# Kernel optimization log

Hardware: AMD Instinct MI355X
Metric: run time of the kernel (lower is better)

The kernel has to match this reference:

```python
import jax, jax.numpy as jnp
import numpy as np

B, N, E = 4, 10000, 160000
F_EXOG = 8
IN_DIM = 9          # 1 (pm25) + F_EXOG
HIST, PRED = 8, 12
HID = 64
GNN_OUT = 13
E_HID, E_OUT = 32, 30
GRU_IN = IN_DIM + GNN_OUT  # 22


def setup_inputs() -> dict:
    key = jax.random.key(0)
    ks = jax.random.split(key, 16)
    s = 0.1
    return {
        "pm25_hist": jax.random.normal(ks[0], (B, HIST, N, 1), jnp.float32),
        "feature": jax.random.normal(ks[1], (B, HIST + PRED, N, F_EXOG), jnp.float32),
        "edge_attr": jax.random.uniform(ks[2], (E, 2), jnp.float32),
        "wind_mean": jnp.array([2.0, 180.0], jnp.float32),
        "wind_std": jnp.array([1.5, 90.0], jnp.float32),
        # edge MLP: Linear(21->32), Sigmoid, Linear(32->30), Sigmoid
        "e_w1": jax.random.normal(ks[3], (2 * IN_DIM + 3, E_HID), jnp.float32) * s,
        "e_b1": jnp.zeros((E_HID,), jnp.float32),
        "e_w2": jax.random.normal(ks[4], (E_HID, E_OUT), jnp.float32) * s,
        "e_b2": jnp.zeros((E_OUT,), jnp.float32),
        # node MLP: Linear(30->13), Sigmoid
        "n_w": jax.random.normal(ks[5], (E_OUT, GNN_OUT), jnp.float32) * s,
        "n_b": jnp.zeros((GNN_OUT,), jnp.float32),
        # GRUCell(22 -> 64), torch layout: weight_ih (3H, in), weight_hh (3H, H)
        "gru_wi": jax.random.normal(ks[6], (3 * HID, GRU_IN), jnp.float32) * s,
        "gru_wh": jax.random.normal(ks[7], (3 * HID, HID), jnp.float32) * s,
        "gru_bi": jnp.zeros((3 * HID,), jnp.float32),
        "gru_bh": jnp.zeros((3 * HID,), jnp.float32),
        # fc_out: Linear(64 -> 1)
        "fc_w": jax.random.normal(ks[8], (HID, 1), jnp.float32) * s,
        "fc_b": jnp.zeros((1,), jnp.float32),
        "edge_index": jax.random.randint(ks[9], (2, E), 0, N, jnp.int64),
    }


def _forward(pm25_hist, feature, edge_attr, wind_mean, wind_std,
             e_w1, e_b1, e_w2, e_b2, n_w, n_b,
             gru_wi, gru_wh, gru_bi, gru_bh, fc_w, fc_b, edge_index):
    batch, _, n_nodes, _ = pm25_hist.shape
    src, tgt = edge_index[0], edge_index[1]

    # buffers precomputed in __init__ (torch.std uses ddof=1)
    edge_mean = edge_attr.mean(axis=0, keepdims=True)
    edge_std = jnp.maximum(jnp.std(edge_attr, axis=0, ddof=1, keepdims=True), 1e-6)
    edge_attr_norm = (edge_attr - edge_mean) / edge_std          # (E, 2)
    city_dist = jnp.maximum(edge_attr[:, 0], 1e-3)               # (E,)
    city_direc = edge_attr[:, 1]                                 # (E,)
    w_std = jnp.maximum(wind_std, 1e-6)

    def graph_gnn(x):                                            # x: (B, N, IN_DIM)
        node_src = x[:, src]                                     # (B, E, IN_DIM)
        node_tgt = x[:, tgt]
        wind = node_src[..., -2:] * w_std + wind_mean            # de-normalize
        speed = jnp.maximum(wind[..., 0], 0.0)                   # (B, E)
        wdir = jnp.deg2rad(wind[..., 1])
        theta = jnp.abs(city_direc - wdir)
        edge_w = jax.nn.relu(3.0 * speed * jnp.cos(theta) / city_dist)  # (B, E)
        ean = jnp.broadcast_to(edge_attr_norm, (x.shape[0], E, 2))
        h = jnp.concatenate([node_src, node_tgt, ean, edge_w[..., None]], axis=-1)
        h = jax.nn.sigmoid(h @ e_w1 + e_b1)
        h = jax.nn.sigmoid(h @ e_w2 + e_b2)                      # (B, E, E_OUT)
        agg = jnp.zeros((x.shape[0], n_nodes, E_OUT), x.dtype)
        agg = agg.at[:, tgt].add(h).at[:, src].add(-h)           # scatter add / sub
        return jax.nn.sigmoid(agg @ n_w + n_b)                   # (B, N, GNN_OUT)

    def gru_step(h, x):                                          # h,x: (B*N, .)
        gi = x @ gru_wi.T + gru_bi
        gh = h @ gru_wh.T + gru_bh
        i_r, i_z, i_n = jnp.split(gi, 3, axis=-1)
        h_r, h_z, h_n = jnp.split(gh, 3, axis=-1)
        r = jax.nn.sigmoid(i_r + h_r)
        z = jax.nn.sigmoid(i_z + h_z)
        n = jnp.tanh(i_n + r * h_n)
        return (1.0 - z) * n + z * h

    def step(carry, feat_t):
        hn, xn = carry                                           # (B*N,HID), (B,N,1)
        x = jnp.concatenate([xn, feat_t], axis=-1)               # (B, N, IN_DIM)
        x_gnn = graph_gnn(x)
        xc = jnp.concatenate([x_gnn, x], axis=-1).reshape(batch * n_nodes, -1)
        hn = gru_step(hn, xc)
        xn = hn.reshape(batch, n_nodes, HID) @ fc_w + fc_b       # (B, N, 1)
        return (hn, xn), xn[..., 0]

    hn0 = jnp.zeros((batch * n_nodes, HID), pm25_hist.dtype)
    xn0 = pm25_hist[:, -1]                                       # (B, N, 1)
    feats = jnp.swapaxes(feature[:, HIST:HIST + PRED], 0, 1)     # (PRED, B, N, F)
    _, preds = jax.lax.scan(step, (hn0, xn0), feats)             # (PRED, B, N)
    return jnp.transpose(preds, (1, 2, 0))                       # (B, N, PRED)


def reference(pm25_hist, feature, edge_attr, wind_mean, wind_std,
              e_w1, e_b1, e_w2, e_b2, n_w, n_b,
              gru_wi, gru_wh, gru_bi, gru_bh, fc_w, fc_b, edge_index):
    return _forward(pm25_hist, feature, edge_attr, wind_mean, wind_std,
                    e_w1, e_b1, e_w2, e_b2, n_w, n_b,
                    gru_wi, gru_wh, gru_bi, gru_bh, fc_w, fc_b, edge_index)
```

## Files before the change

### kernel.cpp

```cpp
#include <hip/hip_runtime.h>
#include <hip/hip_fp16.h>
#include <cstddef>

#define BB    4
#define NN    10000
#define EE    160000
#define BN    40000
#define HISTC 8
#define PREDC 12
#define TSTEP 20
#define FEX   8
#define HIDC  64
#define EHID  32
#define EOUTC 30
#define GOUTC 13
#define GINC  22

typedef float v2f __attribute__((ext_vector_type(2)));
typedef _Float16 v2h __attribute__((ext_vector_type(2)));
typedef _Float16 v8h __attribute__((ext_vector_type(8)));
typedef float f32x4 __attribute__((ext_vector_type(4)));

__device__ __forceinline__ float fast_rcp(float x) { return __builtin_amdgcn_rcpf(x); }
__device__ __forceinline__ float sigm(float x) {
    return fast_rcp(1.0f + __expf(-x));
}
__device__ __forceinline__ v2f sigm2(v2f x) {
    v2f r; r.x = sigm(x.x); r.y = sigm(x.y); return r;
}
__device__ __forceinline__ float tanh_fast(float x) {
    x = fminf(fmaxf(x, -15.0f), 15.0f);
    float e = __expf(2.0f * x);
    return (e - 1.0f) * fast_rcp(e + 1.0f);
}

__device__ __forceinline__ float dot2(__half2 a, __half2 b, float c) {
#if __has_builtin(__builtin_amdgcn_fdot2)
    union { __half2 h; v2h v; } ua, ub;
    ua.h = a; ub.h = b;
    return __builtin_amdgcn_fdot2(ua.v, ub.v, c, false);
#else
    float2 fa = __half22float2(a), fb = __half22float2(b);
    return c + fa.x * fb.x + fa.y * fb.y;
#endif
}

__global__ __launch_bounds__(256) void stats1_kernel(const float* __restrict__ ea,
                                                     double* __restrict__ part) {
    __shared__ double sm[256][4];
    int tid = threadIdx.x;
    double s0 = 0, s1 = 0, q0 = 0, q1 = 0;
    for (int e = blockIdx.x * 256 + tid; e < EE; e += 256 * 256) {
        float2 v = reinterpret_cast<const float2*>(ea)[e];
        double v0 = (double)v.x, v1 = (double)v.y;
        s0 += v0; q0 += v0 * v0;
        s1 += v1; q1 += v1 * v1;
    }
    sm[tid][0] = s0; sm[tid][1] = s1; sm[tid][2] = q0; sm[tid][3] = q1;
    __syncthreads();
    for (int off = 128; off > 0; off >>= 1) {
        if (tid < off)
            for (int k = 0; k < 4; k++) sm[tid][k] += sm[tid + off][k];
        __syncthreads();
    }
    if (tid == 0) {
        part[blockIdx.x * 4 + 0] = sm[0][0];
        part[blockIdx.x * 4 + 1] = sm[0][1];
        part[blockIdx.x * 4 + 2] = sm[0][2];
        part[blockIdx.x * 4 + 3] = sm[0][3];
    }
}

__global__ __launch_bounds__(256) void stats2_kernel(const double* __restrict__ part,
                                                     float* __restrict__ stats) {
    __shared__ double sm[256][4];
    int tid = threadIdx.x;
    sm[tid][0] = part[tid * 4 + 0];
    sm[tid][1] = part[tid * 4 + 1];
    sm[tid][2] = part[tid * 4 + 2];
    sm[tid][3] = part[tid * 4 + 3];
    __syncthreads();
    for (int off = 128; off > 0; off >>= 1) {
        if (tid < off)
            for (int k = 0; k < 4; k++) sm[tid][k] += sm[tid + off][k];
        __syncthreads();
    }
    if (tid == 0) {
        double m0 = sm[0][0] / EE, m1 = sm[0][1] / EE;
        double v0 = (sm[0][2] - sm[0][0] * sm[0][0] / EE) / (double)(EE - 1);
        double v1 = (sm[0][3] - sm[0][1] * sm[0][1] / EE) / (double)(EE - 1);
        float sd0 = fmaxf((float)sqrt(v0 > 0 ? v0 : 0.0), 1e-6f);
        float sd1 = fmaxf((float)sqrt(v1 > 0 ? v1 : 0.0), 1e-6f);
        stats[0] = (float)m0; stats[1] = (float)m1;
        stats[2] = 1.0f / sd0; stats[3] = 1.0f / sd1;
    }
}

__global__ __launch_bounds__(256) void edgepre_kernel(
    const float* __restrict__ ea, const float* __restrict__ stats,
    const int* __restrict__ eidx,
    int* __restrict__ deg_t, int* __restrict__ deg_s,
    float4* __restrict__ epre4)
{
    int e = blockIdx.x * 256 + threadIdx.x;
    if (e >= EE) return;
    float2 v = reinterpret_cast<const float2*>(ea)[e];
    float4 r;
    r.x = (v.x - stats[0]) * stats[2];
    r.y = (v.y - stats[1]) * stats[3];
    r.z = 1.0f / fmaxf(v.x, 1e-3f);
    r.w = v.y;
    epre4[e] = r;
    atomicAdd(&deg_s[eidx[e]], 1);
    atomicAdd(&deg_t[eidx[EE + e]], 1);
}

__global__ __launch_bounds__(256) void cvtw_kernel(
    const float* __restrict__ wi, const float* __restrict__ wh,
    const float* __restrict__ ew2, const float* __restrict__ eb2,
    const float* __restrict__ nw,
    __half* __restrict__ wi_h, __half* __restrict__ wh_h,
    __half* __restrict__ w2b, __half* __restrict__ nwb)
{
    int i = blockIdx.x * 256 + threadIdx.x;
    if (i < 192 * GINC) wi_h[i] = __float2half(wi[i]);
    if (i < 192 * HIDC) wh_h[i] = __float2half(wh[i]);
    if (i < 32 * 32) {
        int o = i >> 5, k = i & 31;
        w2b[i] = (o < EOUTC) ? __float2half(ew2[k * EOUTC + o]) : __half(0.0f);
    }
    if (i < 16 * 32) {
        int j = i >> 5, o = i & 31;
        nwb[i] = (j < GOUTC && o < EOUTC) ? __float2half(nw[o * GOUTC + j])
                                          : __half(0.0f);
    }
}

__global__ void initxn_kernel(const float* __restrict__ pm, float* __restrict__ xn) {
    int i = blockIdx.x * 256 + threadIdx.x;
    if (i >= BN) return;
    int b = i / NN, n = i - b * NN;
    xn[i] = pm[(b * HISTC + (HISTC - 1)) * NN + n];
}

__global__ __launch_bounds__(1024) void scan_kernel(
    const int* __restrict__ deg_t, const int* __restrict__ deg_s,
    int* __restrict__ off_t, int* __restrict__ off_s,
    int* __restrict__ cnt_t, int* __restrict__ cnt_s)
{
    __shared__ int pt[1024], ps[1024];
    int tid = threadIdx.x;
    int base = tid * 10;
    int st = 0, ss = 0;
    for (int k = 0; k < 10; k++) {
        int i = base + k;
        if (i < NN) { st += deg_t[i]; ss += deg_s[i]; }
    }
    pt[tid] = st; ps[tid] = ss;
    __syncthreads();
    for (int off = 1; off < 1024; off <<= 1) {
        int vt = (tid >= off) ? pt[tid - off] : 0;
        int vs = (tid >= off) ? ps[tid - off] : 0;
        __syncthreads();
        pt[tid] += vt; ps[tid] += vs;
        __syncthreads();
    }
    int ext = (tid == 0) ? 0 : pt[tid - 1];
    int exs = (tid == 0) ? 0 : ps[tid - 1];
    for (int k = 0; k < 10; k++) {
        int i = base + k;
        if (i < NN) {
            off_t[i] = ext; cnt_t[i] = ext;
            off_s[i] = exs; cnt_s[i] = exs;
            ext += deg_t[i]; exs += deg_s[i];
        }
    }
    if (tid == 0) { off_t[NN] = EE; off_s[NN] = EE; }
}

__global__ void fillperm_kernel(const int* __restrict__ eidx,
                                const float4* __restrict__ epre4,
                                int* __restrict__ cnt_t, int* __restrict__ cnt_s,
                                int4* __restrict__ eT, float4* __restrict__ epreT)
{
    int e = blockIdx.x * 256 + threadIdx.x;
    if (e >= EE) return;
    int s = eidx[e];
    int g = eidx[EE + e];
    int pt = atomicAdd(&cnt_t[g], 1);
    int ps = atomicAdd(&cnt_s[s], 1);
    int4 r; r.x = s; r.y = g; r.z = ps; r.w = 0;
    eT[pt] = r;
    epreT[pt] = epre4[e];
}

__global__ __launch_bounds__(256) void pre_kernel(
    float* __restrict__ xncur, const float* __restrict__ feature, int t,
    const float* __restrict__ xp,
    const float* __restrict__ fb,
    const float* __restrict__ ew1,
    const float* __restrict__ wmean, const float* __restrict__ wstd,
    __half* __restrict__ preS, __half* __restrict__ preT,
    float2* __restrict__ wind2, float* __restrict__ out)
{
    __shared__ alignas(16) float w1s[18 * EHID];
    for (int i = threadIdx.x; i < 18 * EHID; i += 256) w1s[i] = ew1[i];
    __syncthreads();
    int idx = blockIdx.x * 256 + threadIdx.x;
    if (idx >= BN * 8) return;
    int i = idx >> 3;
    int c = idx & 7;
    int b = i / NN, n = i - b * NN;
    float x0;
    if (t == 0) {
        x0 = xncur[i];
    } else {
        x0 = (xp[i] + xp[BN + i]) + (xp[2 * BN + i] + xp[3 * BN + i]) + fb[0];
        if (c == 0) {
            xncur[i] = x0;
            out[(size_t)i * PREDC + (t - 1)] = x0;
        }
    }
    float x[9];
    x[0] = x0;
    {
        const float4* fp = reinterpret_cast<const float4*>(
            feature + (((size_t)b * TSTEP + HISTC + t) * NN + n) * FEX);
        float4 u = fp[0], v = fp[1];
        x[1] = u.x; x[2] = u.y; x[3] = u.z; x[4] = u.w;
        x[5] = v.x; x[6] = v.y; x[7] = v.z; x[8] = v.w;
    }
    float4 aS = {0.f, 0.f, 0.f, 0.f}, aT = {0.f, 0.f, 0.f, 0.f};
    #pragma unroll
    for (int k = 0; k < 9; k++) {
        float4 wS = reinterpret_cast<const float4*>(&w1s[k * EHID])[c];
        float4 wT = reinterpret_cast<const float4*>(&w1s[(9 + k) * EHID])[c];
        aS.x += x[k] * wS.x; aS.y += x[k] * wS.y; aS.z += x[k] * wS.z; aS.w += x[k] * wS.w;
        aT.x += x[k] * wT.x; aT.y += x[k] * wT.y; aT.z += x[k] * wT.z; aT.w += x[k] * wT.w;
    }
    union { uint2 u; __half h[4]; } sv, tv;
    sv.h[0] = __float2half(aS.x); sv.h[1] = __float2half(aS.y);
    sv.h[2] = __float2half(aS.z); sv.h[3] = __float2half(aS.w);
    tv.h[0] = __float2half(aT.x); tv.h[1] = __float2half(aT.y);
    tv.h[2] = __float2half(aT.z); tv.h[3] = __float2half(aT.w);
    reinterpret_cast<uint2*>(preS + (size_t)i * EHID)[c] = sv.u;
    reinterpret_cast<uint2*>(preT + (size_t)i * EHID)[c] = tv.u;
    if (c == 1) {
        float sd0 = fmaxf(wstd[0], 1e-6f), sd1 = fmaxf(wstd[1], 1e-6f);
        float speed = fmaxf(x[7] * sd0 + wmean[0], 0.f);
        float wdir  = (x[8] * sd1 + wmean[1]) * 0.017453292519943295f;
        float2 wv; wv.x = 3.0f * speed; wv.y = wdir;
        wind2[i] = wv;
    }
}

__global__ __launch_bounds__(256) void finalout_kernel(
    const float* __restrict__ xp, const float* __restrict__ fb,
    float* __restrict__ out)
{
    int i = blockIdx.x * 256 + threadIdx.x;
    if (i >= BN) return;
    out[(size_t)i * PREDC + (PREDC - 1)] =
        (xp[i] + xp[BN + i]) + (xp[2 * BN + i] + xp[3 * BN + i]) + fb[0];
}

#define H1STR 40
#define S2STR 36
#define H3STR 20
__global__ __launch_bounds__(256) void edge_kernel(
    const int4* __restrict__ eT, const float4* __restrict__ epreT,
    const __half* __restrict__ preS, const __half* __restrict__ preT,
    const float2* __restrict__ wind2,
    const float* __restrict__ ew1, const float* __restrict__ eb1,
    const __half* __restrict__ w2b, const __half* __restrict__ nwb,
    const float* __restrict__ eb2,
    __half* __restrict__ h3t, __half* __restrict__ h3s)
{
    __shared__ alignas(16) __half h1s[256 * H1STR];
    __shared__ alignas(16) __half s2s[4][16 * S2STR];
    __shared__ alignas(16) __half h3x[256 * H3STR];

    int tid  = threadIdx.x;
    int lane = tid & 63, wv = tid >> 6;
    int l15  = lane & 15, lk = lane >> 4;
    int i = blockIdx.x * 256 + tid;
    int b = blockIdx.y;
    int4 et = eT[i];
    int s = et.x, g = et.y, ps = et.z;
    float4 ep = epreT[i];

    size_t iS = (size_t)b * NN + s, iT = (size_t)b * NN + g;
    float2 wvd = wind2[iS];
    float ew = fmaxf(wvd.x * __cosf(fabsf(ep.w - wvd.y)) * ep.z, 0.f);

    v8h bw2a, bw2b, bnw;
    {
        union { uint4 u; v8h h; } t;
        t.u = *reinterpret_cast<const uint4*>(w2b + l15 * 32 + lk * 8);        bw2a = t.h;
        t.u = *reinterpret_cast<const uint4*>(w2b + (16 + l15) * 32 + lk * 8); bw2b = t.h;
        t.u = *reinterpret_cast<const uint4*>(nwb + l15 * 32 + lk * 8);        bnw  = t.h;
    }
    float b2v0 = eb2[l15];
    float b2v1 = eb2[(16 + l15) < EOUTC ? (16 + l15) : (EOUTC - 1)];

    union alignas(16) { uint4 u[4]; __half2 h2[16]; } RS, RT;
    {
        const uint4* p;
        p = reinterpret_cast<const uint4*>(preS + iS * EHID);
        RS.u[0] = p[0]; RS.u[1] = p[1]; RS.u[2] = p[2]; RS.u[3] = p[3];
        p = reinterpret_cast<const uint4*>(preT + iT * EHID);
        RT.u[0] = p[0]; RT.u[1] = p[1]; RT.u[2] = p[2]; RT.u[3] = p[3];
    }

    const v2f* W18 = reinterpret_cast<const v2f*>(ew1 + 18 * EHID);
    const v2f* W19 = reinterpret_cast<const v2f*>(ew1 + 19 * EHID);
    const v2f* W20 = reinterpret_cast<const v2f*>(ew1 + 20 * EHID);
    const v2f* B1  = reinterpret_cast<const v2f*>(eb1);
    float ean0 = ep.x, ean1 = ep.y;
    union alignas(16) { uint4 u[4]; __half2 h2[16]; } H1;
    #pragma unroll
    for (int q = 0; q < 16; q++) {
        v2f u = W18[q] * ean0 + W19[q] * ean1 + B1[q] + W20[q] * ew;
        float2 rs = __half22float2(RS.h2[q]);
        float2 rt = __half22float2(RT.h2[q]);
        u.x += rs.x + rt.x;
        u.y += rs.y + rt.y;
        v2f sg = sigm2(u);
        H1.h2[q] = __floats2half2_rn(sg.x, sg.y);
    }
    {
        uint4* dst = reinterpret_cast<uint4*>(h1s + tid * H1STR);
        dst[0] = H1.u[0]; dst[1] = H1.u[1]; dst[2] = H1.u[2]; dst[3] = H1.u[3];
    }

    f32x4 zero = {0.f, 0.f, 0.f, 0.f};
    __half* s2w = s2s[wv];
    #pragma unroll
    for (int mt = 0; mt < 4; ++mt) {
        v8h af;
        {
            union { uint4 u; v8h h; } t;
            t.u = *reinterpret_cast<const uint4*>(
                h1s + (wv * 64 + mt * 16 + l15) * H1STR + lk * 8);
            af = t.h;
        }
        f32x4 a0 = __builtin_amdgcn_mfma_f32_16x16x32_f16(af, bw2a, zero, 0, 0, 0);
        f32x4 a1 = __builtin_amdgcn_mfma_f32_16x16x32_f16(af, bw2b, zero, 0, 0, 0);
        #pragma unroll
        for (int q = 0; q < 4; ++q) {
            int rl = lk * 4 + q;
            s2w[rl * S2STR + l15]      = __float2half(sigm(a0[q] + b2v0));
            s2w[rl * S2STR + 16 + l15] = __float2half(sigm(a1[q] + b2v1));
        }
        v8h a2;
        {
            union { uint2 u[2]; v8h h; } t;
            const __half* p2 = s2w + l15 * S2STR + lk * 8;
            t.u[0] = *reinterpret_cast<const uint2*>(p2);
            t.u[1] = *reinterpret_cast<const uint2*>(p2 + 4);
            a2 = t.h;
        }
        f32x4 h3a = __builtin_amdgcn_mfma_f32_16x16x32_f16(a2, bnw, zero, 0, 0, 0);
        #pragma unroll
        for (int q = 0; q < 4; ++q) {
            h3x[(wv * 64 + mt * 16 + lk * 4 + q) * H3STR + l15] = __float2half(h3a[q]);
        }
    }

    union alignas(16) { uint4 u4[2]; uint2 u[4]; } R;
    {
        const uint2* hp = reinterpret_cast<const uint2*>(h3x + tid * H3STR);
        R.u[0] = hp[0]; R.u[1] = hp[1]; R.u[2] = hp[2]; R.u[3] = hp[3];
    }
    {
        __half* oT = h3t + ((size_t)b * EE + i) * 16;
        reinterpret_cast<uint4*>(oT)[0] = R.u4[0];
        reinterpret_cast<uint4*>(oT)[1] = R.u4[1];
        __half* oS = h3s + ((size_t)b * EE + ps) * 16;
        reinterpret_cast<uint4*>(oS)[0] = R.u4[0];
        reinterpret_cast<uint4*>(oS)[1] = R.u4[1];
    }
}

__global__ __launch_bounds__(256) void gather_kernel(
    const __half* __restrict__ h3t, const __half* __restrict__ h3s,
    const int* __restrict__ off_t, const int* __restrict__ off_s,
    const float* __restrict__ nb, const float* __restrict__ xncur,
    __half* __restrict__ xcagg)
{
    int n = (blockIdx.x * 256 + threadIdx.x) >> 6;
    if (n >= NN) return;
    n = __builtin_amdgcn_readfirstlane(n);
    int lane = threadIdx.x & 63;
    int b   = lane >> 4;
    int e4  = (lane >> 2) & 3;
    int chq = lane & 3;

    const __half* ht = h3t + (size_t)b * ((size_t)EE * 16) + chq * 4;
    const __half* hs = h3s + (size_t)b * ((size_t)EE * 16) + chq * 4;

    float a0 = 0.f, a1 = 0.f, a2 = 0.f, a3 = 0.f;
    {
        int i0 = off_t[n], i1 = off_t[n + 1];
        for (int i = i0 + e4; i < i1; i += 4) {
            uint2 v = *reinterpret_cast<const uint2*>(ht + (size_t)i * 16);
            float2 f01 = __half22float2(*reinterpret_cast<__half2*>(&v.x));
            float2 f23 = __half22float2(*reinterpret_cast<__half2*>(&v.y));
            a0 += f01.x; a1 += f01.y; a2 += f23.x; a3 += f23.y;
        }
    }
    {
        int i0 = off_s[n], i1 = off_s[n + 1];
        for (int i = i0 + e4; i < i1; i += 4) {
            uint2 v = *reinterpret_cast<const uint2*>(hs + (size_t)i * 16);
            float2 f01 = __half22float2(*reinterpret_cast<__half2*>(&v.x));
            float2 f23 = __half22float2(*reinterpret_cast<__half2*>(&v.y));
            a0 -= f01.x; a1 -= f01.y; a2 -= f23.x; a3 -= f23.y;
        }
    }
    a0 += __shfl_xor(a0, 4); a1 += __shfl_xor(a1, 4);
    a2 += __shfl_xor(a2, 4); a3 += __shfl_xor(a3, 4);
    a0 += __shfl_xor(a0, 8); a1 += __shfl_xor(a1, 8);
    a2 += __shfl_xor(a2, 8); a3 += __shfl_xor(a3, 8);

    if (e4 == 0) {
        int c0 = chq * 4;
        float nb0 = nb[c0 < GOUTC ? c0 : GOUTC - 1];
        float nb1 = nb[c0 + 1 < GOUTC ? c0 + 1 : GOUTC - 1];
        float nb2 = nb[c0 + 2 < GOUTC ? c0 + 2 : GOUTC - 1];
        float nb3 = nb[c0 + 3 < GOUTC ? c0 + 3 : GOUTC - 1];
        float v0 = (c0 + 0 < GOUTC) ? sigm(a0 + nb0) : 0.f;
        float v1 = (c0 + 1 < GOUTC) ? sigm(a1 + nb1)
                 : ((c0 + 1 == GOUTC) ? xncur[(size_t)b * NN + n] : 0.f);
        float v2 = (c0 + 2 < GOUTC) ? sigm(a2 + nb2) : 0.f;
        float v3 = (c0 + 3 < GOUTC) ? sigm(a3 + nb3) : 0.f;
        union { uint2 u; __half h[4]; } o;
        o.h[0] = __float2half(v0); o.h[1] = __float2half(v1);
        o.h[2] = __float2half(v2); o.h[3] = __float2half(v3);
        *reinterpret_cast<uint2*>(xcagg + ((size_t)b * NN + n) * 16 + c0) = o.u;
    }
}

__global__ __launch_bounds__(256) void node_kernel(
    const __half* __restrict__ xcagg, const float* __restrict__ feature, int t,
    const __half* __restrict__ wi_h, const __half* __restrict__ wh_h,
    const float* __restrict__ bi, const float* __restrict__ bh,
    const float* __restrict__ fw,
    const __half2* __restrict__ hnold, __half2* __restrict__ hnnew,
    float* __restrict__ xp)
{
    __shared__ float xpart[4][64];
    int lane = threadIdx.x & 63;
    int wav  = threadIdx.x >> 6;
    int jb   = blockIdx.y;
    int node = blockIdx.x * 64 + lane;
    int b = node / NN;
    int n = node - b * NN;

    __half2 xch[11];
    {
        union alignas(16) { uint4 u[2]; __half2 h2[8]; } X;
        const uint4* xp16 = reinterpret_cast<const uint4*>(xcagg + (size_t)node * 16);
        X.u[0] = xp16[0]; X.u[1] = xp16[1];
        #pragma unroll
        for (int p = 0; p < 7; p++) xch[p] = X.h2[p];
    }
    {
        const float4* fp = reinterpret_cast<const float4*>(
            feature + (((size_t)b * TSTEP + HISTC + t) * NN + n) * FEX);
        float4 u = fp[0], v = fp[1];
        xch[7]  = __floats2half2_rn(u.x, u.y);
        xch[8]  = __floats2half2_rn(u.z, u.w);
        xch[9]  = __floats2half2_rn(v.x, v.y);
        xch[10] = __floats2half2_rn(v.z, v.w);
    }

    __half2 hh[32];
    #pragma unroll
    for (int p = 0; p < 32; p++) hh[p] = hnold[(size_t)p * BN + node];

    float xsum = 0.f;
    #pragma unroll
    for (int jj2 = 0; jj2 < 2; jj2++) {
        int j0 = __builtin_amdgcn_readfirstlane(jb * 16 + wav * 4 + jj2 * 2);
        union { __half2 h; __half v[2]; } holdw;
        holdw.h = hnold[(size_t)(j0 >> 1) * BN + node];
        float hnew2[2];
        #pragma unroll
        for (int d = 0; d < 2; d++) {
            int j = j0 + d;
            float ir = bi[j], iz = bi[64 + j], in_ = bi[128 + j];
            const __half2* wr0 = reinterpret_cast<const __half2*>(wi_h + (size_t)j * GINC);
            const __half2* wr1 = reinterpret_cast<const __half2*>(wi_h + (size_t)(64 + j) * GINC);
            const __half2* wr2 = reinterpret_cast<const __half2*>(wi_h + (size_t)(128 + j) * GINC);
            #pragma unroll
            for (int p = 0; p < 11; p++) {
                ir  = dot2(xch[p], wr0[p], ir);
                iz  = dot2(xch[p], wr1[p], iz);
                in_ = dot2(xch[p], wr2[p], in_);
            }
            float hr0 = bh[j], hz0 = bh[64 + j], hn0 = bh[128 + j];
            float hr1 = 0.f, hz1 = 0.f, hn1 = 0.f;
            const __half2* vr0 = reinterpret_cast<const __half2*>(wh_h + (size_t)j * HIDC);
            const __half2* vr1 = reinterpret_cast<const __half2*>(wh_h + (size_t)(64 + j) * HIDC);
            const __half2* vr2 = reinterpret_cast<const __half2*>(wh_h + (size_t)(128 + j) * HIDC);
            #pragma unroll
            for (int p = 0; p < 32; p += 2) {
                hr0 = dot2(hh[p],     vr0[p],     hr0);
                hz0 = dot2(hh[p],     vr1[p],     hz0);
                hn0 = dot2(hh[p],     vr2[p],     hn0);
                hr1 = dot2(hh[p + 1], vr0[p + 1], hr1);
                hz1 = dot2(hh[p + 1], vr1[p + 1], hz1);
                hn1 = dot2(hh[p + 1], vr2[p + 1], hn1);
            }
            float r  = sigm(ir + hr0 + hr1);
            float z  = sigm(iz + hz0 + hz1);
            float nn = tanh_fast(in_ + r * (hn0 + hn1));
            float hold = __half2float(holdw.v[d]);
            float hnew = (1.f - z) * nn + z * hold;
            hnew2[d] = hnew;
            xsum += hnew * fw[j];
        }
        hnnew[(size_t)(j0 >> 1) * BN + node] = __floats2half2_rn(hnew2[0], hnew2[1]);
    }
    xpart[wav][lane] = xsum;
    __syncthreads();
    if (wav == 0) {
        float tot = xpart[0][lane] + xpart[1][lane] + xpart[2][lane] + xpart[3][lane];
        xp[(size_t)jb * BN + node] = tot;
    }
}

extern "C" void kernel_launch(void* const* d_in, const int* in_sizes, int n_in,
                              void* d_out, int out_size, void* d_ws, size_t ws_size,
                              hipStream_t stream)
{
    const float* pm    = (const float*)d_in[0];
    const float* feat  = (const float*)d_in[1];
    const float* ea    = (const float*)d_in[2];
    const float* wmean = (const float*)d_in[3];
    const float* wstd  = (const float*)d_in[4];
    const float* ew1   = (const float*)d_in[5];
    const float* eb1   = (const float*)d_in[6];
    const float* ew2   = (const float*)d_in[7];
    const float* eb2   = (const float*)d_in[8];
    const float* nw    = (const float*)d_in[9];
    const float* nb    = (const float*)d_in[10];
    const float* wi    = (const float*)d_in[11];
    const float* wh    = (const float*)d_in[12];
    const float* bi    = (const float*)d_in[13];
    const float* bh    = (const float*)d_in[14];
    const float* fw    = (const float*)d_in[15];
    const float* fb    = (const float*)d_in[16];
    const int*   eidx  = (const int*)d_in[17];
    float* out = (float*)d_out;

    char* w = (char*)d_ws;
    double* partd = (double*)w;                    w += 256 * 4 * sizeof(double);
    float*  stats = (float*)w;                     w += 16 * sizeof(float);
    float4* epre4 = (float4*)w;                    w += (size_t)EE * sizeof(float4);
    float4* epreT = (float4*)w;                    w += (size_t)EE * sizeof(float4);
    float*  xncur = (float*)w;                     w += (size_t)BN * sizeof(float);
    float*  xp    = (float*)w;                     w += (size_t)4 * BN * sizeof(float);
    __half2* hnA  = (__half2*)w;                   w += (size_t)32 * BN * sizeof(__half2);
    __half2* hnB  = (__half2*)w;                   w += (size_t)32 * BN * sizeof(__half2);
    __half* xcagg = (__half*)w;                    w += (size_t)BN * 16 * sizeof(__half);
    __half* preS  = (__half*)w;                    w += (size_t)BN * EHID * sizeof(__half);
    __half* preT  = (__half*)w;                    w += (size_t)BN * EHID * sizeof(__half);
    float2* wind2 = (float2*)w;                    w += (size_t)BN * sizeof(float2);
    __half* h3t   = (__half*)w;                    w += (size_t)BB * EE * 16 * sizeof(__half);
    __half* h3s   = (__half*)w;                    w += (size_t)BB * EE * 16 * sizeof(__half);
    __half* wi_h  = (__half*)w;                    w += (size_t)192 * GINC * sizeof(__half);
    __half* wh_h  = (__half*)w;                    w += (size_t)192 * HIDC * sizeof(__half);
    __half* w2b   = (__half*)w;                    w += (size_t)32 * 32 * sizeof(__half);
    __half* nwb   = (__half*)w;                    w += (size_t)16 * 32 * sizeof(__half);
    int*    deg_t = (int*)w;                       w += NN * sizeof(int);
    int*    deg_s = (int*)w;                       w += NN * sizeof(int);
    int*    off_t = (int*)w;                       w += (NN + 1) * sizeof(int);
    int*    off_s = (int*)w;                       w += (NN + 1) * sizeof(int);
    int*    cnt_t = (int*)w;                       w += NN * sizeof(int);
    int*    cnt_s = (int*)w;                       w += NN * sizeof(int);
    int4*   eT    = (int4*)w;                      w += (size_t)EE * sizeof(int4);

    stats1_kernel<<<256, 256, 0, stream>>>(ea, partd);
    stats2_kernel<<<1, 256, 0, stream>>>(partd, stats);
    hipMemsetAsync(deg_t, 0, 2 * NN * sizeof(int), stream);
    edgepre_kernel<<<(EE + 255) / 256, 256, 0, stream>>>(
        ea, stats, eidx, deg_t, deg_s, epre4);
    cvtw_kernel<<<(192 * HIDC + 255) / 256, 256, 0, stream>>>(
        wi, wh, ew2, eb2, nw, wi_h, wh_h, w2b, nwb);
    initxn_kernel<<<(BN + 255) / 256, 256, 0, stream>>>(pm, xncur);
    hipMemsetAsync(hnA, 0, (size_t)32 * BN * sizeof(__half2), stream);
    scan_kernel<<<1, 1024, 0, stream>>>(deg_t, deg_s, off_t, off_s, cnt_t, cnt_s);
    fillperm_kernel<<<(EE + 255) / 256, 256, 0, stream>>>(
        eidx, epre4, cnt_t, cnt_s, eT, epreT);

    for (int t = 0; t < PREDC; t++) {
        const __half2* hnold = (t & 1) ? hnB : hnA;
        __half2*       hnnew = (t & 1) ? hnA : hnB;
        pre_kernel<<<(BN * 8 + 255) / 256, 256, 0, stream>>>(
            xncur, feat, t, xp, fb, ew1, wmean, wstd, preS, preT, wind2, out);
        edge_kernel<<<dim3(EE / 256, BB), 256, 0, stream>>>(
            eT, epreT, preS, preT, wind2, ew1, eb1, w2b, nwb, eb2, h3t, h3s);
        gather_kernel<<<(NN * 64 + 255) / 256, 256, 0, stream>>>(
            h3t, h3s, off_t, off_s, nb, xncur, xcagg);
        node_kernel<<<dim3(BN / 64, 4), 256, 0, stream>>>(
            xcagg, feat, t, wi_h, wh_h, bi, bh, fw, hnold, hnnew, xp);
    }
    finalout_kernel<<<(BN + 255) / 256, 256, 0, stream>>>(xp, fb, out);
}
```

Before: 929.8 us.

## Reduce target-side edge messages in-block with atomics instead of writing h3t

The edge kernel now relies on edges being sorted by target: each block sums its 256 edge outputs per target node from shared memory and atomically adds them into a small float aggT buffer. The separate h3t global array and the gather kernel's target-side loop go away. The gather kernel reads aggT and zeroes it for the next step. This cuts a large per-step global write and read stream. The cost is an extra block barrier, atomics at block-boundary nodes, and a serial per-node loop inside each block.

```diff
diff --git a/kernel.cpp b/kernel.cpp
--- a/kernel.cpp
+++ b/kernel.cpp
@@ -274,11 +274,13 @@
     const float* __restrict__ ew1, const float* __restrict__ eb1,
     const __half* __restrict__ w2b, const __half* __restrict__ nwb,
     const float* __restrict__ eb2,
-    __half* __restrict__ h3t, __half* __restrict__ h3s)
+    const int* __restrict__ off_t,
+    __half* __restrict__ h3s, float* __restrict__ aggT)
 {
     __shared__ alignas(16) __half h1s[256 * H1STR];
     __shared__ alignas(16) __half s2s[4][16 * S2STR];
     __shared__ alignas(16) __half h3x[256 * H3STR];
+    __shared__ int gseg[2];
 
     int tid  = threadIdx.x;
     int lane = tid & 63, wv = tid >> 6;
@@ -288,6 +290,8 @@
     int4 et = eT[i];
     int s = et.x, g = et.y, ps = et.z;
     float4 ep = epreT[i];
+    if (tid == 0)   gseg[0] = g;
+    if (tid == 255) gseg[1] = g;
 
     size_t iS = (size_t)b * NN + s, iT = (size_t)b * NN + g;
     float2 wvd = wind2[iS];
@@ -366,25 +370,40 @@
             h3x[(wv * 64 + mt * 16 + lk * 4 + q) * H3STR + l15] = __float2half(h3a[q]);
         }
     }
-
-    union alignas(16) { uint4 u4[2]; uint2 u[4]; } R;
-    {
+    __syncthreads();
+
+    {
+        union alignas(16) { uint4 u4[2]; uint2 u[4]; } R;
         const uint2* hp = reinterpret_cast<const uint2*>(h3x + tid * H3STR);
         R.u[0] = hp[0]; R.u[1] = hp[1]; R.u[2] = hp[2]; R.u[3] = hp[3];
-    }
-    {
-        __half* oT = h3t + ((size_t)b * EE + i) * 16;
-        reinterpret_cast<uint4*>(oT)[0] = R.u4[0];
-        reinterpret_cast<uint4*>(oT)[1] = R.u4[1];
         __half* oS = h3s + ((size_t)b * EE + ps) * 16;
         reinterpret_cast<uint4*>(oS)[0] = R.u4[0];
         reinterpret_cast<uint4*>(oS)[1] = R.u4[1];
     }
+
+    {
+        int base = blockIdx.x * 256;
+        int g0 = gseg[0], g1 = gseg[1];
+        int ch = tid & 15;
+        for (int nl = tid >> 4; g0 + nl <= g1; nl += 16) {
+            int node = g0 + nl;
+            int lo = off_t[node], hi = off_t[node + 1];
+            lo = lo < base ? base : lo;
+            int lim = base + 256;
+            hi = hi > lim ? lim : hi;
+            if (ch < GOUTC && lo < hi) {
+                float sum = 0.f;
+                for (int sx = lo; sx < hi; ++sx)
+                    sum += __half2float(h3x[(sx - base) * H3STR + ch]);
+                atomicAdd(&aggT[((size_t)b * NN + node) * 16 + ch], sum);
+            }
+        }
+    }
 }
 
 __global__ __launch_bounds__(256) void gather_kernel(
-    const __half* __restrict__ h3t, const __half* __restrict__ h3s,
-    const int* __restrict__ off_t, const int* __restrict__ off_s,
+    const __half* __restrict__ h3s, float* __restrict__ aggT,
+    const int* __restrict__ off_s,
     const float* __restrict__ nb, const float* __restrict__ xncur,
     __half* __restrict__ xcagg)
 {
@@ -396,19 +415,9 @@
     int e4  = (lane >> 2) & 3;
     int chq = lane & 3;
 
-    const __half* ht = h3t + (size_t)b * ((size_t)EE * 16) + chq * 4;
     const __half* hs = h3s + (size_t)b * ((size_t)EE * 16) + chq * 4;
 
     float a0 = 0.f, a1 = 0.f, a2 = 0.f, a3 = 0.f;
-    {
-        int i0 = off_t[n], i1 = off_t[n + 1];
-        for (int i = i0 + e4; i < i1; i += 4) {
-            uint2 v = *reinterpret_cast<const uint2*>(ht + (size_t)i * 16);
-            float2 f01 = __half22float2(*reinterpret_cast<__half2*>(&v.x));
-            float2 f23 = __half22float2(*reinterpret_cast<__half2*>(&v.y));
-            a0 += f01.x; a1 += f01.y; a2 += f23.x; a3 += f23.y;
-        }
-    }
     {
         int i0 = off_s[n], i1 = off_s[n + 1];
         for (int i = i0 + e4; i < i1; i += 4) {
@@ -425,15 +434,19 @@
 
     if (e4 == 0) {
         int c0 = chq * 4;
+        float* ap = aggT + ((size_t)b * NN + n) * 16 + c0;
+        float4 av = *reinterpret_cast<const float4*>(ap);
+        float4 z4 = {0.f, 0.f, 0.f, 0.f};
+        *reinterpret_cast<float4*>(ap) = z4;
         float nb0 = nb[c0 < GOUTC ? c0 : GOUTC - 1];
         float nb1 = nb[c0 + 1 < GOUTC ? c0 + 1 : GOUTC - 1];
         float nb2 = nb[c0 + 2 < GOUTC ? c0 + 2 : GOUTC - 1];
         float nb3 = nb[c0 + 3 < GOUTC ? c0 + 3 : GOUTC - 1];
-        float v0 = (c0 + 0 < GOUTC) ? sigm(a0 + nb0) : 0.f;
-        float v1 = (c0 + 1 < GOUTC) ? sigm(a1 + nb1)
+        float v0 = (c0 + 0 < GOUTC) ? sigm(a0 + av.x + nb0) : 0.f;
+        float v1 = (c0 + 1 < GOUTC) ? sigm(a1 + av.y + nb1)
                  : ((c0 + 1 == GOUTC) ? xncur[(size_t)b * NN + n] : 0.f);
-        float v2 = (c0 + 2 < GOUTC) ? sigm(a2 + nb2) : 0.f;
-        float v3 = (c0 + 3 < GOUTC) ? sigm(a3 + nb3) : 0.f;
+        float v2 = (c0 + 2 < GOUTC) ? sigm(a2 + av.z + nb2) : 0.f;
+        float v3 = (c0 + 3 < GOUTC) ? sigm(a3 + av.w + nb3) : 0.f;
         union { uint2 u; __half h[4]; } o;
         o.h[0] = __float2half(v0); o.h[1] = __float2half(v1);
         o.h[2] = __float2half(v2); o.h[3] = __float2half(v3);
@@ -568,8 +581,8 @@
     __half* preS  = (__half*)w;                    w += (size_t)BN * EHID * sizeof(__half);
     __half* preT  = (__half*)w;                    w += (size_t)BN * EHID * sizeof(__half);
     float2* wind2 = (float2*)w;                    w += (size_t)BN * sizeof(float2);
-    __half* h3t   = (__half*)w;                    w += (size_t)BB * EE * 16 * sizeof(__half);
     __half* h3s   = (__half*)w;                    w += (size_t)BB * EE * 16 * sizeof(__half);
+    float*  aggT  = (float*)w;                     w += (size_t)BN * 16 * sizeof(float);
     __half* wi_h  = (__half*)w;                    w += (size_t)192 * GINC * sizeof(__half);
     __half* wh_h  = (__half*)w;                    w += (size_t)192 * HIDC * sizeof(__half);
     __half* w2b   = (__half*)w;                    w += (size_t)32 * 32 * sizeof(__half);
@@ -585,6 +598,7 @@
     stats1_kernel<<<256, 256, 0, stream>>>(ea, partd);
     stats2_kernel<<<1, 256, 0, stream>>>(partd, stats);
     hipMemsetAsync(deg_t, 0, 2 * NN * sizeof(int), stream);
+    hipMemsetAsync(aggT, 0, (size_t)BN * 16 * sizeof(float), stream);
     edgepre_kernel<<<(EE + 255) / 256, 256, 0, stream>>>(
         ea, stats, eidx, deg_t, deg_s, epre4);
     cvtw_kernel<<<(192 * HIDC + 255) / 256, 256, 0, stream>>>(
@@ -601,9 +615,10 @@
         pre_kernel<<<(BN * 8 + 255) / 256, 256, 0, stream>>>(
             xncur, feat, t, xp, fb, ew1, wmean, wstd, preS, preT, wind2, out);
         edge_kernel<<<dim3(EE / 256, BB), 256, 0, stream>>>(
-            eT, epreT, preS, preT, wind2, ew1, eb1, w2b, nwb, eb2, h3t, h3s);
+            eT, epreT, preS, preT, wind2, ew1, eb1, w2b, nwb, eb2,
+            off_t, h3s, aggT);
         gather_kernel<<<(NN * 64 + 255) / 256, 256, 0, stream>>>(
-            h3t, h3s, off_t, off_s, nb, xncur, xcagg);
+            h3s, aggT, off_s, nb, xncur, xcagg);
         node_kernel<<<dim3(BN / 64, 4), 256, 0, stream>>>(
             xcagg, feat, t, wi_h, wh_h, bi, bh, fw, hnold, hnnew, xp);
     }
```

Result: no change. 929.6 us (-0.0%).
